# Optimization experiments

Hardware: AMD Instinct MI355X
Metric: run time of the kernel (lower is better)

Reference implementation:

```python
import jax, jax.numpy as jnp
from jax import lax
import numpy as np

START = 1  # strings_utils.SpecialSymbol.START
B, T, H, V = 16, 256, 512, 32000


def setup_inputs() -> dict:
    key = jax.random.key(0)
    ks = jax.random.split(key, 8)
    s = 0.05
    return {
        "hidden0": jax.random.normal(ks[0], (1, B, H), jnp.float32),
        "target": jax.random.randint(ks[1], (B, T), 0, V, jnp.int32),
        "E": jax.random.normal(ks[2], (V, H), jnp.float32) * s,
        "W_ih": jax.random.normal(ks[3], (3 * H, H), jnp.float32) * s,
        "W_hh": jax.random.normal(ks[4], (3 * H, H), jnp.float32) * s,
        "b_ih": jax.random.normal(ks[5], (3 * H,), jnp.float32) * s,
        "b_hh": jax.random.normal(ks[6], (3 * H,), jnp.float32) * s,
        "b_out": jax.random.normal(ks[7], (V,), jnp.float32) * s,
    }


def reference(hidden0, target, E, W_ih, W_hh, b_ih, b_hh, b_out):
    # Teacher forcing: step 0 feeds START, step di>0 feeds target[:, di-1]
    b, t = target.shape
    start = jnp.full((b, 1), START, dtype=target.dtype)
    step_tok = jnp.concatenate([start, target[:, :-1]], axis=1).T  # [T, B]
    h0 = hidden0[0]  # num_layers == 1 -> [B, H]

    def step(h, tok):
        x = E[tok]                                # [B, H] embedding gather
        gi = x @ W_ih.T + b_ih                    # [B, 3H]
        gh = h @ W_hh.T + b_hh                    # [B, 3H]
        i_r, i_z, i_n = jnp.split(gi, 3, axis=-1)
        h_r, h_z, h_n = jnp.split(gh, 3, axis=-1)
        r = jax.nn.sigmoid(i_r + h_r)
        z = jax.nn.sigmoid(i_z + h_z)
        n = jnp.tanh(i_n + r * h_n)
        h_new = (1.0 - z) * n + z * h             # [B, H]
        logits = h_new @ E.T + b_out              # tied-weight output [B, V]
        return h_new, logits

    _, logits = lax.scan(step, h0, step_tok)      # [T, B, V]
    return jnp.transpose(logits, (1, 0, 2))       # [B, T, V]
```

## Files before the change

### kernel.cpp

```cpp
#include <hip/hip_runtime.h>
#include <hip/hip_bf16.h>
#include <math.h>

#define Bq 16
#define Tq 256
#define Hq 512
#define Vq 32000
#define Gq 1536
#define NWG 16
#define LBLK 240
#define NBI 167
#define NTILES (32 * NBI)

typedef __attribute__((ext_vector_type(8))) short short8;
typedef __attribute__((ext_vector_type(4))) float f32x4;
typedef __attribute__((ext_vector_type(4))) unsigned int u32x4;
typedef unsigned long long u64;

typedef const __attribute__((address_space(1))) void g_void;
typedef __attribute__((address_space(3))) void l_void;

__device__ __forceinline__ unsigned short f2bf(float f) {
    union { float f; unsigned int u; } v; v.f = f;
    unsigned int r = v.u + 0x7fffu + ((v.u >> 16) & 1u);
    return (unsigned short)(r >> 16);
}
__device__ __forceinline__ float bf2f(unsigned short h) {
    union { unsigned int u; float f; } v; v.u = ((unsigned int)h) << 16;
    return v.f;
}
__device__ __forceinline__ float sigm(float x) { return 1.0f / (1.0f + __expf(-x)); }
__device__ __forceinline__ float tanh_fast(float x) {
    float e = __expf(-2.0f * x);
    return (1.0f - e) / (1.0f + e);
}

__launch_bounds__(384)
__global__ void prep_gi_kernel(const int* __restrict__ target, const float* __restrict__ E,
                               const float* __restrict__ Wih, const float* __restrict__ Whh,
                               const float* __restrict__ b_ih,
                               unsigned short* __restrict__ Ebf,
                               unsigned short* __restrict__ WhhHi,
                               unsigned short* __restrict__ WhhLo,
                               float* __restrict__ gi_all,
                               int* __restrict__ flags) {
    int bid = blockIdx.x, tid = threadIdx.x;
    if (bid >= 4096) {
        long g = (long)(bid - 4096) * 384 + tid;
        long stride = 1536L * 384;
        for (long i = g; i < (long)Vq * Hq; i += stride) Ebf[i] = f2bf(E[i]);
        for (long i = g; i < (long)Gq * Hq; i += stride) {
            float w = Whh[i]; unsigned short hi = f2bf(w);
            WhhHi[i] = hi; WhhLo[i] = f2bf(w - bf2f(hi));
        }
        if (g < 2048) flags[g] = 0;
        return;
    }
    __shared__ __align__(16) unsigned short Ahi[16][520];
    __shared__ __align__(16) unsigned short Alo[16][520];
    __shared__ int toks[16];
    int t = bid >> 4, gb = bid & 15;
    if (tid < 16) toks[tid] = (t == 0) ? 1 : target[tid * Tq + (t - 1)];
    __syncthreads();
    for (int idx = tid; idx < 16 * Hq; idx += 384) {
        int r = idx >> 9, k = idx & 511;
        float v = E[(long)toks[r] * Hq + k];
        unsigned short hi = f2bf(v);
        Ahi[r][k] = hi; Alo[r][k] = f2bf(v - bf2f(hi));
    }
    __syncthreads();
    int wave = tid >> 6, lane = tid & 63;
    int gcb = gb * 96 + wave * 16;
    int row = lane & 15, kg = (lane >> 4) * 8;
    const float* wrow = Wih + (long)(gcb + row) * Hq;
    f32x4 aHH = {0,0,0,0}, aHL = {0,0,0,0}, aLH = {0,0,0,0};
#pragma unroll
    for (int ks = 0; ks < 16; ++ks) {
        int k0 = ks * 32 + kg;
        short8 ah = *(const short8*)&Ahi[row][k0];
        short8 al = *(const short8*)&Alo[row][k0];
        f32x4 wa = *(const f32x4*)&wrow[k0];
        f32x4 wb = *(const f32x4*)&wrow[k0 + 4];
        short8 wh, wl;
#pragma unroll
        for (int e = 0; e < 4; ++e) {
            unsigned short hi = f2bf(wa[e]);
            wh[e] = (short)hi; wl[e] = (short)f2bf(wa[e] - bf2f(hi));
            hi = f2bf(wb[e]);
            wh[e + 4] = (short)hi; wl[e + 4] = (short)f2bf(wb[e] - bf2f(hi));
        }
        aHH = __builtin_amdgcn_mfma_f32_16x16x32_bf16(ah, wh, aHH, 0, 0, 0);
        aHL = __builtin_amdgcn_mfma_f32_16x16x32_bf16(ah, wl, aHL, 0, 0, 0);
        aLH = __builtin_amdgcn_mfma_f32_16x16x32_bf16(al, wh, aLH, 0, 0, 0);
    }
    int g = gcb + row;
    float bi = b_ih[g];
#pragma unroll
    for (int q = 0; q < 4; ++q) {
        int b = (lane >> 4) * 4 + q;
        gi_all[((long)(t * 16 + b)) * Gq + g] = aHH[q] + aHL[q] + aLH[q] + bi;
    }
}

__launch_bounds__(384, 1)
__global__ void fused_kernel(const float* __restrict__ h0,
                             const unsigned short* __restrict__ WhhHi,
                             const unsigned short* __restrict__ WhhLo,
                             const float* __restrict__ b_hh,
                             const float* __restrict__ gi_all,
                             unsigned int* Hpk,
                             int* flags,
                             const unsigned short* __restrict__ Ebf,
                             const float* __restrict__ b_out,
                             float* __restrict__ out) {
    __shared__ __align__(16) char smem[41984];
    int tid = threadIdx.x, lane = tid & 63;

    if (blockIdx.x < NWG) {
        __builtin_amdgcn_s_setprio(1);
        unsigned short (*Ahi)[520] = (unsigned short (*)[520])smem;
        float (*gbuf)[16][33] = (float (*)[16][33])(smem + 16640);
        int w = blockIdx.x;
        int wave = tid >> 6;
        int gate = wave >> 1;
        int gcol = gate * 512 + w * 32 + (wave & 1) * 16;
        int row = lane & 15, kg = (lane >> 4) * 8;
        const unsigned short* bhp = WhhHi + (long)(gcol + row) * Hq;
        const unsigned short* blp = WhhLo + (long)(gcol + row) * Hq;
        short8 Bh[16], Bl[16];
#pragma unroll
        for (int ks = 0; ks < 16; ++ks) {
            Bh[ks] = *(const short8*)&bhp[ks * 32 + kg];
            Bl[ks] = *(const short8*)&blp[ks * 32 + kg];
        }
        float bhh = b_hh[gcol + row];
        float gin[4];
#pragma unroll
        for (int q = 0; q < 4; ++q) {
            int b = (lane >> 4) * 4 + q;
            gin[q] = gi_all[(long)b * Gq + (gcol + row)];
        }
        for (int t = 0; t < Tq; ++t) {
            if (t == 0) {
                for (int idx = tid; idx < Bq * Hq; idx += 384)
                    Ahi[idx >> 9][idx & 511] = f2bf(h0[idx]);
            } else {
                int guard = 0;
                while (guard < (1 << 15)) {
                    int fv = __hip_atomic_load(&flags[lane * 32], __ATOMIC_RELAXED,
                                               __HIP_MEMORY_SCOPE_AGENT);
                    if (__all(fv >= t)) break;
                    __builtin_amdgcn_s_sleep(1);
                    ++guard;
                }
                asm volatile("" ::: "memory");
                const u32x4* src = (const u32x4*)(Hpk + (long)(t - 1) * 4096);
                u32x4 v0 = src[tid];
                u32x4 v1 = src[tid + 384];
                u32x4 v2 = (tid < 256) ? src[tid + 768] : v0;
                {
                    int c = tid;
                    *(u32x4*)&Ahi[c >> 6][((c * 4) & 255) * 2] = v0;
                    c = tid + 384;
                    *(u32x4*)&Ahi[c >> 6][((c * 4) & 255) * 2] = v1;
                    if (tid < 256) {
                        c = tid + 768;
                        *(u32x4*)&Ahi[c >> 6][((c * 4) & 255) * 2] = v2;
                    }
                }
            }
            __syncthreads();
            f32x4 xH = {0,0,0,0}, xL = {0,0,0,0};
            f32x4 yH = {0,0,0,0}, yL = {0,0,0,0};
#pragma unroll
            for (int ks = 0; ks < 8; ++ks) {
                short8 ah = *(const short8*)&Ahi[row][ks * 32 + kg];
                xH = __builtin_amdgcn_mfma_f32_16x16x32_bf16(ah, Bh[ks], xH, 0, 0, 0);
                xL = __builtin_amdgcn_mfma_f32_16x16x32_bf16(ah, Bl[ks], xL, 0, 0, 0);
            }
#pragma unroll
            for (int ks = 8; ks < 16; ++ks) {
                short8 ah = *(const short8*)&Ahi[row][ks * 32 + kg];
                yH = __builtin_amdgcn_mfma_f32_16x16x32_bf16(ah, Bh[ks], yH, 0, 0, 0);
                yL = __builtin_amdgcn_mfma_f32_16x16x32_bf16(ah, Bl[ks], yL, 0, 0, 0);
            }
            int jj = (wave & 1) * 16 + row;
#pragma unroll
            for (int q = 0; q < 4; ++q) {
                int b = (lane >> 4) * 4 + q;
                float ghv = (xH[q] + yH[q]) + (xL[q] + yL[q]) + bhh;
                if (gate < 2) gbuf[gate][b][jj] = ghv + gin[q];
                else { gbuf[2][b][jj] = gin[q]; gbuf[3][b][jj] = ghv; }
            }
            __syncthreads();
            if (tid < 256) {
                int b = tid >> 4, jp = tid & 15;
                int j0 = jp * 2, j1 = j0 + 1;
                int jc0 = w * 32 + j0;
                float r0 = sigm(gbuf[0][b][j0]);
                float z0 = sigm(gbuf[1][b][j0]);
                float n0 = tanh_fast(gbuf[2][b][j0] + r0 * gbuf[3][b][j0]);
                float hn0 = (1.0f - z0) * n0 + z0 * bf2f(Ahi[b][jc0]);
                float r1 = sigm(gbuf[0][b][j1]);
                float z1 = sigm(gbuf[1][b][j1]);
                float n1 = tanh_fast(gbuf[2][b][j1] + r1 * gbuf[3][b][j1]);
                float hn1 = (1.0f - z1) * n1 + z1 * bf2f(Ahi[b][jc0 + 1]);
                unsigned int pk = (unsigned int)f2bf(hn0) |
                                  ((unsigned int)f2bf(hn1) << 16);
                __hip_atomic_store(&Hpk[(long)t * 4096 + b * 256 + w * 16 + jp], pk,
                                   __ATOMIC_RELAXED, __HIP_MEMORY_SCOPE_AGENT);
                asm volatile("s_waitcnt vmcnt(0)" ::: "memory");
                if (lane == 0)
                    __hip_atomic_store(&flags[(w * 4 + wave) * 32], t + 1,
                                       __ATOMIC_RELAXED, __HIP_MEMORY_SCOPE_AGENT);
            }
            int tp = (t + 1 < Tq) ? (t + 1) : t;
#pragma unroll
            for (int q = 0; q < 4; ++q) {
                int b = (lane >> 4) * 4 + q;
                gin[q] = gi_all[((long)(tp * 16 + b)) * Gq + (gcol + row)];
            }
        }
    } else {
        unsigned short* As = (unsigned short*)smem;
        unsigned short* Bs = As + 128 * 64;
        int slot = blockIdx.x - NWG;
        int wid = tid >> 6;
        int wr = wid & 1, wc = wid >> 1;
        int fr = lane & 15, r7 = lane & 7, sb = lane >> 4;
        int rA = lane >> 3, slp = (lane & 7) ^ rA;
        for (int tile = slot; tile < NTILES; tile += LBLK) {
            int mt = tile / NBI, nbi = tile % NBI;
            int m0 = mt * 128, n0 = nbi * 192;
            if (tid < 64) {
                int need = (mt + 1) * 8;
                int guard = 0;
                while (guard < (1 << 18)) {
                    int fv = __hip_atomic_load(&flags[lane * 32], __ATOMIC_RELAXED,
                                               __HIP_MEMORY_SCOPE_AGENT);
                    if (__all(fv >= need)) break;
                    __builtin_amdgcn_s_sleep(127);
                    ++guard;
                }
            }
            __syncthreads();
            f32x4 acc[4][4] = {};
            const unsigned int* srcA = Hpk + (long)(mt * 8) * 4096;
            for (int kt = 0; kt < 8; ++kt) {
                if (kt) __syncthreads();
                int ko = kt * 64;
#pragma unroll
                for (int i = 0; i < 4; ++i) {
                    int brow = n0 + wid * 8 + i * 48 + rA;
                    if (brow > Vq - 1) brow = Vq - 1;
                    __builtin_amdgcn_global_load_lds(
                        (g_void*)(Ebf + (long)brow * Hq + ko + slp * 8),
                        (l_void*)(Bs + (wid * 8 + i * 48) * 64), 16, 0, 0);
                }
                for (int c = tid; c < 1024; c += 384) {
                    int r = c >> 3, g8 = c & 7;
                    u32x4 v = *(const u32x4*)&srcA[(long)(r >> 4) * 4096 +
                                                   (r & 15) * 256 + kt * 32 + g8 * 4];
                    *(u32x4*)&As[r * 64 + ((g8 ^ (r & 7)) << 3)] = v;
                }
                __syncthreads();
#pragma unroll
                for (int ks = 0; ks < 2; ++ks) {
                    short8 af[4], bfr[4];
#pragma unroll
                    for (int f = 0; f < 4; ++f) {
                        af[f]  = *(const short8*)&As[(wr * 64 + f * 16 + fr) * 64 +
                                                     (((sb + ks * 4) ^ r7) << 3)];
                        bfr[f] = *(const short8*)&Bs[(wc * 64 + f * 16 + fr) * 64 +
                                                     (((sb + ks * 4) ^ r7) << 3)];
                    }
#pragma unroll
                    for (int fm = 0; fm < 4; ++fm)
#pragma unroll
                        for (int fn = 0; fn < 4; ++fn)
                            acc[fm][fn] = __builtin_amdgcn_mfma_f32_16x16x32_bf16(
                                af[fm], bfr[fn], acc[fm][fn], 0, 0, 0);
                }
            }
#pragma unroll
            for (int fn = 0; fn < 4; ++fn) {
                int v = n0 + wc * 64 + fn * 16 + fr;
                if (v < Vq) {
                    float bo = b_out[v];
#pragma unroll
                    for (int fm = 0; fm < 4; ++fm) {
#pragma unroll
                        for (int q = 0; q < 4; ++q) {
                            int m = m0 + wr * 64 + fm * 16 + (lane >> 4) * 4 + q;
                            out[((long)(m & 15) * Tq + (m >> 4)) * Vq + v] =
                                acc[fm][fn][q] + bo;
                        }
                    }
                }
            }
        }
    }
}

extern "C" void kernel_launch(void* const* d_in, const int* in_sizes, int n_in,
                              void* d_out, int out_size, void* d_ws, size_t ws_size,
                              hipStream_t stream) {
    const float* h0    = (const float*)d_in[0];
    const int*   target= (const int*)d_in[1];
    const float* E     = (const float*)d_in[2];
    const float* Wih   = (const float*)d_in[3];
    const float* Whh   = (const float*)d_in[4];
    const float* b_ih  = (const float*)d_in[5];
    const float* b_hh  = (const float*)d_in[6];
    const float* b_out = (const float*)d_in[7];
    float* out = (float*)d_out;

    char* ws = (char*)d_ws;
    size_t off = 0;
    unsigned short* Ebf   = (unsigned short*)(ws + off); off += (size_t)Vq * Hq * 2;
    unsigned short* WhhHi = (unsigned short*)(ws + off); off += (size_t)Gq * Hq * 2;
    unsigned short* WhhLo = (unsigned short*)(ws + off); off += (size_t)Gq * Hq * 2;
    float*          gi_all= (float*)(ws + off);          off += (size_t)Tq * Bq * Gq * 4;
    unsigned int*   Hpk   = (unsigned int*)(ws + off);   off += (size_t)Tq * 4096 * 4;
    int*            flags = (int*)(ws + off);            off += 2048 * 4;

    prep_gi_kernel<<<dim3(5632), dim3(384), 0, stream>>>(target, E, Wih, Whh, b_ih,
                                                         Ebf, WhhHi, WhhLo, gi_all,
                                                         flags);
    fused_kernel<<<dim3(256), dim3(384), 0, stream>>>(h0, WhhHi, WhhLo, b_hh, gi_all,
                                                      Hpk, flags, Ebf, b_out, out);
}
```

Before: 1.045 ms.

## Replace flag-based step sync with tagged double-buffered hidden-state ring

Each hidden-state element is published as a 64-bit word tagged with its step number in a two-slot ring, so consumers poll the data itself instead of a separate flag array. This removes the store-then-waitcnt-then-flag round trip on the recurrent critical path. Flags are now written only every 8 steps, presumably for the logits blocks that read Hpk. The cost is twice the global traffic per step on the ring and more polling loads. Reusing two slots relies on no workgroup getting more than one step ahead of the others.

```diff
diff --git a/kernel.cpp b/kernel.cpp
--- a/kernel.cpp
+++ b/kernel.cpp
@@ -108,7 +108,7 @@
                              const unsigned short* __restrict__ WhhLo,
                              const float* __restrict__ b_hh,
                              const float* __restrict__ gi_all,
-                             unsigned int* Hpk,
+                             unsigned int* Hpk, u64* ring,
                              int* flags,
                              const unsigned short* __restrict__ Ebf,
                              const float* __restrict__ b_out,
@@ -145,28 +145,33 @@
                 for (int idx = tid; idx < Bq * Hq; idx += 384)
                     Ahi[idx >> 9][idx & 511] = f2bf(h0[idx]);
             } else {
+                const u64* src = ring + ((t - 1) & 1) * 4096;
+                u64 vb[11];
+                bool ok;
                 int guard = 0;
-                while (guard < (1 << 15)) {
-                    int fv = __hip_atomic_load(&flags[lane * 32], __ATOMIC_RELAXED,
-                                               __HIP_MEMORY_SCOPE_AGENT);
-                    if (__all(fv >= t)) break;
-                    __builtin_amdgcn_s_sleep(1);
-                    ++guard;
-                }
-                asm volatile("" ::: "memory");
-                const u32x4* src = (const u32x4*)(Hpk + (long)(t - 1) * 4096);
-                u32x4 v0 = src[tid];
-                u32x4 v1 = src[tid + 384];
-                u32x4 v2 = (tid < 256) ? src[tid + 768] : v0;
-                {
-                    int c = tid;
-                    *(u32x4*)&Ahi[c >> 6][((c * 4) & 255) * 2] = v0;
-                    c = tid + 384;
-                    *(u32x4*)&Ahi[c >> 6][((c * 4) & 255) * 2] = v1;
-                    if (tid < 256) {
-                        c = tid + 768;
-                        *(u32x4*)&Ahi[c >> 6][((c * 4) & 255) * 2] = v2;
-                    }
+                do {
+#pragma unroll
+                    for (int k = 0; k < 10; ++k)
+                        vb[k] = __hip_atomic_load(&src[tid + k * 384], __ATOMIC_RELAXED,
+                                                  __HIP_MEMORY_SCOPE_AGENT);
+                    vb[10] = (tid < 256)
+                        ? __hip_atomic_load(&src[3840 + tid], __ATOMIC_RELAXED,
+                                            __HIP_MEMORY_SCOPE_AGENT)
+                        : ((u64)(unsigned int)t << 32);
+                    ok = true;
+#pragma unroll
+                    for (int k = 0; k < 11; ++k)
+                        ok = ok && ((unsigned int)(vb[k] >> 32) == (unsigned int)t);
+                    if (!ok) __builtin_amdgcn_s_sleep(1);
+                } while (!ok && ++guard < (1 << 15));
+#pragma unroll
+                for (int k = 0; k < 10; ++k) {
+                    int wv = tid + k * 384;
+                    *(unsigned int*)&Ahi[wv >> 8][(wv & 255) * 2] = (unsigned int)vb[k];
+                }
+                if (tid < 256) {
+                    int wv = 3840 + tid;
+                    *(unsigned int*)&Ahi[wv >> 8][(wv & 255) * 2] = (unsigned int)vb[10];
                 }
             }
             __syncthreads();
@@ -207,12 +212,18 @@
                 float hn1 = (1.0f - z1) * n1 + z1 * bf2f(Ahi[b][jc0 + 1]);
                 unsigned int pk = (unsigned int)f2bf(hn0) |
                                   ((unsigned int)f2bf(hn1) << 16);
-                __hip_atomic_store(&Hpk[(long)t * 4096 + b * 256 + w * 16 + jp], pk,
+                long idx = b * 256 + w * 16 + jp;
+                u64 word = ((u64)(unsigned int)(t + 1) << 32) | pk;
+                __hip_atomic_store(&ring[(t & 1) * 4096 + idx], word,
                                    __ATOMIC_RELAXED, __HIP_MEMORY_SCOPE_AGENT);
-                asm volatile("s_waitcnt vmcnt(0)" ::: "memory");
-                if (lane == 0)
-                    __hip_atomic_store(&flags[(w * 4 + wave) * 32], t + 1,
-                                       __ATOMIC_RELAXED, __HIP_MEMORY_SCOPE_AGENT);
+                __hip_atomic_store(&Hpk[(long)t * 4096 + idx], pk,
+                                   __ATOMIC_RELAXED, __HIP_MEMORY_SCOPE_AGENT);
+                if ((t & 7) == 7) {
+                    asm volatile("s_waitcnt vmcnt(0)" ::: "memory");
+                    if (lane == 0)
+                        __hip_atomic_store(&flags[(w * 4 + wave) * 32], t + 1,
+                                           __ATOMIC_RELAXED, __HIP_MEMORY_SCOPE_AGENT);
+                }
             }
             int tp = (t + 1 < Tq) ? (t + 1) : t;
 #pragma unroll
@@ -322,11 +333,12 @@
     unsigned short* WhhLo = (unsigned short*)(ws + off); off += (size_t)Gq * Hq * 2;
     float*          gi_all= (float*)(ws + off);          off += (size_t)Tq * Bq * Gq * 4;
     unsigned int*   Hpk   = (unsigned int*)(ws + off);   off += (size_t)Tq * 4096 * 4;
+    u64*            ring  = (u64*)(ws + off);            off += (size_t)2 * 4096 * 8;
     int*            flags = (int*)(ws + off);            off += 2048 * 4;
 
     prep_gi_kernel<<<dim3(5632), dim3(384), 0, stream>>>(target, E, Wih, Whh, b_ih,
                                                          Ebf, WhhHi, WhhLo, gi_all,
                                                          flags);
     fused_kernel<<<dim3(256), dim3(384), 0, stream>>>(h0, WhhHi, WhhLo, b_hh, gi_all,
-                                                      Hpk, flags, Ebf, b_out, out);
-}
+                                                      Hpk, ring, flags, Ebf, b_out, out);
+}
```

Result: faster. 926.4 us (-11.3%).
